# Performance work log

Measured on AMD Instinct MI355X. Metric: run time of the kernel, lower is better.

Reference implementation:

```python
import jax, jax.numpy as jnp
import numpy as np

HEADS = 16
HEAD_DIM = 64
DIM = 1024
INNER = HEADS * HEAD_DIM
EPS = 1e-5


def setup_inputs() -> dict:
    key = jax.random.key(0)
    ks = jax.random.split(key, 7)
    s_qkv = (2.0 / (DIM + 3 * INNER)) ** 0.5
    s_out = (2.0 / (INNER + DIM)) ** 0.5
    return {
        "x": jax.random.normal(ks[0], (4, 2048, DIM), dtype=jnp.float32),
        "w_qkv": jax.random.normal(ks[1], (DIM, 3 * INNER), dtype=jnp.float32) * s_qkv,
        "b_qkv": jnp.zeros((3 * INNER,), dtype=jnp.float32),
        "w_out": jax.random.normal(ks[2], (INNER, DIM), dtype=jnp.float32) * s_out,
        "b_out": jnp.zeros((DIM,), dtype=jnp.float32),
        "ln_gamma": jnp.ones((DIM,), dtype=jnp.float32),
        "ln_beta": jnp.zeros((DIM,), dtype=jnp.float32),
    }


def reference(x, w_qkv, b_qkv, w_out, b_out, ln_gamma, ln_beta):
    # Pre-norm LayerNorm
    mu = jnp.mean(x, axis=-1, keepdims=True)
    var = jnp.var(x, axis=-1, keepdims=True)
    xn = (x - mu) * jax.lax.rsqrt(var + EPS) * ln_gamma + ln_beta
    # QKV projection: [b, l, 3*inner]
    qkv = xn @ w_qkv + b_qkv
    q, k, v = jnp.split(qkv, 3, axis=-1)
    b, l, _ = x.shape
    def heads(t):  # [b, l, inner] -> [b, h, l, d]
        return t.reshape(b, l, HEADS, HEAD_DIM).transpose(0, 2, 1, 3)
    q, k, v = heads(q), heads(k), heads(v)
    scale = HEAD_DIM ** -0.5
    scores = jnp.einsum('bhqd,bhkd->bhqk', q, k) * scale
    att = jax.nn.softmax(scores, axis=-1)
    out = jnp.einsum('bhqk,bhkd->bhqd', att, v)
    out = out.transpose(0, 2, 1, 3).reshape(b, l, INNER)
    return out @ w_out + b_out
```

## Files before the change

kernel.cpp:

```cpp
#include <hip/hip_runtime.h>
#include <stdint.h>

typedef __bf16 bf16;
typedef bf16 bf16x4 __attribute__((ext_vector_type(4)));
typedef bf16 bf16x8 __attribute__((ext_vector_type(8)));
typedef float f32x4 __attribute__((ext_vector_type(4)));


__device__ __forceinline__ void gll16(const bf16* g, const bf16* l) {
  __builtin_amdgcn_global_load_lds(
      (__attribute__((address_space(1))) void*)(g),
      (__attribute__((address_space(3))) void*)(l),
      16, 0, 0);
}

__global__ __launch_bounds__(256) void prep_kernel(
    const float* __restrict__ wqkv, bf16* __restrict__ wqkvT,
    const float* __restrict__ wout, bf16* __restrict__ woutT,
    const float* __restrict__ x, const float* __restrict__ gamma,
    const float* __restrict__ beta, bf16* __restrict__ xn)
{
  __shared__ bf16 tile[32][33];
  __shared__ float red[8];
  const int bid = blockIdx.x;
  const int t = threadIdx.x;
  if (bid < 4096) {
    const int bx = bid & 127, by = bid >> 7;
    const float* in;
    bf16* out;
    int Cc, c0;
    if (bx < 96) { in = wqkv; out = wqkvT; Cc = 3072; c0 = bx * 32; }
    else         { in = wout; out = woutT; Cc = 1024; c0 = (bx - 96) * 32; }
    const int r0 = by * 32;
    const int tx = t & 31, ty = t >> 5;
#pragma unroll
    for (int i = 0; i < 32; i += 8)
      tile[ty + i][tx] = (bf16)in[(long)(r0 + ty + i) * Cc + c0 + tx];
    __syncthreads();
#pragma unroll
    for (int i = 0; i < 32; i += 8)
      out[(long)(c0 + ty + i) * 1024 + r0 + tx] = tile[tx][ty + i];
  } else {
    const long row = bid - 4096;
    f32x4 f = *(const f32x4*)(x + row * 1024 + t * 4);
    float sum = f[0] + f[1] + f[2] + f[3];
    float sq  = f[0]*f[0] + f[1]*f[1] + f[2]*f[2] + f[3]*f[3];
#pragma unroll
    for (int sh = 1; sh < 64; sh <<= 1) {
      sum += __shfl_xor(sum, sh, 64);
      sq  += __shfl_xor(sq,  sh, 64);
    }
    const int wave = t >> 6, lane = t & 63;
    if (lane == 0) { red[wave] = sum; red[wave + 4] = sq; }
    __syncthreads();
    sum = red[0] + red[1] + red[2] + red[3];
    sq  = red[4] + red[5] + red[6] + red[7];
    const float mu  = sum * (1.0f / 1024.0f);
    const float var = sq * (1.0f / 1024.0f) - mu * mu;
    const float rs  = rsqrtf(var + 1e-5f);
    f32x4 g = *(const f32x4*)(gamma + t * 4);
    f32x4 bb = *(const f32x4*)(beta + t * 4);
    bf16x4 ov;
#pragma unroll
    for (int i = 0; i < 4; i++)
      ov[i] = (bf16)((f[i] - mu) * rs * g[i] + bb[i]);
    *(bf16x4*)(xn + row * 1024 + t * 4) = ov;
  }
}

__global__ __launch_bounds__(256, 4) void gemm_bt(
    const bf16* __restrict__ A, const bf16* __restrict__ BT,
    const float* __restrict__ bias, float* __restrict__ C,
    bf16* __restrict__ qb, bf16* __restrict__ kb, bf16* __restrict__ vb,
    int K, int N, int mode)
{
  __shared__ bf16 sA[2][128 * 32];
  __shared__ bf16 sB[2][128 * 32];
  const int t = threadIdx.x;
  const int lane = t & 63;
  const int wave = t >> 6;
  const int wave_u = __builtin_amdgcn_readfirstlane(wave);
  const int quad = lane >> 4;
  const int c16 = lane & 15;
  const int wm = (wave >> 1) * 64;
  const int wn = (wave & 1) * 64;
  const int m0 = blockIdx.x * 128;
  const int n0 = blockIdx.y * 128;

  f32x4 acc[4][4] = {};

  const int srow = t >> 2;
  const int scol = (((t & 3) ^ ((t >> 3) & 3)) * 8);
  const bf16* gA = A + (long)(m0 + srow) * K + scol;
  const bf16* gB = BT + (long)(n0 + srow) * K + scol;
  const long rowskip = (long)64 * K;
  const int ksw = (quad ^ ((c16 >> 1) & 3)) * 8;

  const int S = K >> 5;

  auto stage = [&](int b, int kk) {
    const bf16* lA = sA[0] + b * 4096 + wave_u * 512;
    const bf16* lB = sB[0] + b * 4096 + wave_u * 512;
    const int k0 = kk * 32;
    gll16(gA + k0, lA);
    gll16(gA + k0 + rowskip, lA + 2048);
    gll16(gB + k0, lB);
    gll16(gB + k0 + rowskip, lB + 2048);
  };

  stage(0, 0);

  int cur = 0;
  for (int s = 0; s < S; s++) {
    __syncthreads();
    if (s + 1 < S)
      stage(cur ^ 1, s + 1);
    const bf16* cA = sA[0] + cur * 4096;
    const bf16* cB = sB[0] + cur * 4096;
    bf16x8 af[4], bfr[4];
#pragma unroll
    for (int i = 0; i < 4; i++)
      af[i] = *(const bf16x8*)(cA + (wm + i * 16 + c16) * 32 + ksw);
#pragma unroll
    for (int j = 0; j < 4; j++)
      bfr[j] = *(const bf16x8*)(cB + (wn + j * 16 + c16) * 32 + ksw);
#pragma unroll
    for (int i = 0; i < 4; i++)
#pragma unroll
      for (int j = 0; j < 4; j++)
        acc[i][j] = __builtin_amdgcn_mfma_f32_16x16x32_bf16(af[i], bfr[j], acc[i][j], 0, 0, 0);
    cur ^= 1;
  }

#pragma unroll
  for (int i = 0; i < 4; i++) {
    const int mbase = m0 + wm + i * 16 + quad * 4;
#pragma unroll
    for (int j = 0; j < 4; j++) {
      const int n = n0 + wn + j * 16 + c16;
      const float bv = bias[n];
      if (mode == 0) {
#pragma unroll
        for (int r = 0; r < 4; r++)
          C[(long)(mbase + r) * N + n] = acc[i][j][r] + bv;
      } else {
        const int part = n >> 10;
        const int inner = n & 1023;
        const int h = inner >> 6, d = inner & 63;
        bf16* dst = (part == 0) ? qb : (part == 1) ? kb : vb;
        const float scl = (part == 0) ? 0.18033688f : 1.0f;
#pragma unroll
        for (int r = 0; r < 4; r++) {
          const int m = mbase + r;
          const int b = m >> 11, l = m & 2047;
          const long bh = (long)((b << 4) | h);
          dst[(bh * 2048 + l) * 64 + d] = (bf16)((acc[i][j][r] + bv) * scl);
        }
      }
    }
  }
}

__global__ __launch_bounds__(256, 2) void attn_kernel(
    const bf16* __restrict__ q, const bf16* __restrict__ k,
    const bf16* __restrict__ vb, bf16* __restrict__ att)
{
  __shared__ bf16 sK[128 * 68];
  __shared__ bf16 sVt[64 * 132];

  const int i = blockIdx.x;
  const int xcd = i & 7;
  const int wi = i >> 3;
  const int qt = wi & 7;
  const int bh = xcd * 8 + (wi >> 3);
  const int b = bh >> 4, h = bh & 15;
  const int q0 = qt * 256;
  const int t = threadIdx.x;
  const int wave = t >> 6, lane = t & 63;
  const int quad = lane >> 4, c16 = lane & 15;

  const bf16* qp = q + (long)bh * (2048 * 64);
  const bf16* kp = k + (long)bh * (2048 * 64);
  const bf16* vp = vb + (long)bh * (2048 * 64);

  bf16x8 aq[4][2];
#pragma unroll
  for (int m = 0; m < 4; m++) {
    const bf16* qrow = qp + (long)(q0 + wave * 64 + m * 16 + c16) * 64 + quad * 8;
    aq[m][0] = *(const bf16x8*)(qrow);
    aq[m][1] = *(const bf16x8*)(qrow + 32);
  }

  f32x4 o_acc[4][4] = {};
  f32x4 o_sum[4] = {};
  bf16x8 vones;
#pragma unroll
  for (int z = 0; z < 8; z++) vones[z] = (bf16)1.0f;

  const int kr = t >> 3;
  const int kd = (t & 7) * 8;
  const int lr = t >> 1;
  const int dh = (t & 1) * 32;
  const int l32 = lr & 31;
  const int pcol = (lr >> 5) * 32 + ((l32 >> 2) & 3) * 8 + (l32 >> 4) * 4 + (l32 & 3);

  bf16x8 kreg[4], vreg[4];
#pragma unroll
  for (int it = 0; it < 4; it++)
    kreg[it] = *(const bf16x8*)(kp + (long)(it * 32 + kr) * 64 + kd);
#pragma unroll
  for (int c = 0; c < 4; c++)
    vreg[c] = *(const bf16x8*)(vp + (long)lr * 64 + dh + c * 8);

  for (int kt = 0; kt < 16; kt++) {
    __syncthreads();
#pragma unroll
    for (int it = 0; it < 4; it++)
      *(bf16x8*)&sK[(it * 32 + kr) * 68 + kd] = kreg[it];
#pragma unroll
    for (int c = 0; c < 4; c++)
#pragma unroll
      for (int u = 0; u < 8; u++)
        sVt[(dh + c * 8 + u) * 132 + pcol] = vreg[c][u];
    __syncthreads();

    const int kvn = ((kt + 1) & 15) * 128;

#pragma unroll
    for (int ks = 0; ks < 4; ks++) {
      bf16x8 ap[4];
#pragma unroll
      for (int e = 0; e < 2; e++) {
        const int jb = ks * 2 + e;
        const bf16x8 bk0 = *(const bf16x8*)&sK[(jb * 16 + c16) * 68 + quad * 8];
        const bf16x8 bk1 = *(const bf16x8*)&sK[(jb * 16 + c16) * 68 + 32 + quad * 8];
#pragma unroll
        for (int m = 0; m < 4; m++) {
          f32x4 z = {};
          z = __builtin_amdgcn_mfma_f32_16x16x32_bf16(bk0, aq[m][0], z, 0, 0, 0);
          z = __builtin_amdgcn_mfma_f32_16x16x32_bf16(bk1, aq[m][1], z, 0, 0, 0);
#pragma unroll
          for (int r = 0; r < 4; r++)
            ap[m][e * 4 + r] = (bf16)__builtin_amdgcn_exp2f(z[r]);
        }
      }
      if (ks == 1) {
#pragma unroll
        for (int it = 0; it < 4; it++)
          kreg[it] = *(const bf16x8*)(kp + (long)(kvn + it * 32 + kr) * 64 + kd);
      }
      if (ks == 2) {
#pragma unroll
        for (int c = 0; c < 4; c++)
          vreg[c] = *(const bf16x8*)(vp + (long)(kvn + lr) * 64 + dh + c * 8);
      }
      __builtin_amdgcn_s_setprio(1);
#pragma unroll
      for (int m = 0; m < 4; m++)
        o_sum[m] = __builtin_amdgcn_mfma_f32_16x16x32_bf16(ap[m], vones, o_sum[m], 0, 0, 0);
#pragma unroll
      for (int jd = 0; jd < 4; jd++) {
        const bf16x8 bv = *(const bf16x8*)&sVt[(jd * 16 + c16) * 132 + ks * 32 + quad * 8];
#pragma unroll
        for (int m = 0; m < 4; m++)
          o_acc[m][jd] = __builtin_amdgcn_mfma_f32_16x16x32_bf16(ap[m], bv, o_acc[m][jd], 0, 0, 0);
      }
      __builtin_amdgcn_s_setprio(0);
    }
  }

#pragma unroll
  for (int m = 0; m < 4; m++) {
#pragma unroll
    for (int r = 0; r < 4; r++) {
      const float inv = 1.0f / o_sum[m][r];
      const long rowbase = ((long)b * 2048 + q0 + wave * 64 + m * 16 + quad * 4 + r) * 1024 + h * 64;
#pragma unroll
      for (int jd = 0; jd < 4; jd++)
        att[rowbase + jd * 16 + c16] = (bf16)(o_acc[m][jd][r] * inv);
    }
  }
}

extern "C" void kernel_launch(void* const* d_in, const int* in_sizes, int n_in,
                              void* d_out, int out_size, void* d_ws, size_t ws_size,
                              hipStream_t stream) {
  (void)in_sizes; (void)n_in; (void)out_size; (void)ws_size;
  const float* x     = (const float*)d_in[0];
  const float* w_qkv = (const float*)d_in[1];
  const float* b_qkv = (const float*)d_in[2];
  const float* w_out = (const float*)d_in[3];
  const float* b_out = (const float*)d_in[4];
  const float* gamma = (const float*)d_in[5];
  const float* beta  = (const float*)d_in[6];
  float* out = (float*)d_out;
  bf16* ws  = (bf16*)d_ws;

  bf16* xn    = ws;
  bf16* wqkvT = ws + 8388608;
  bf16* woutT = wqkvT + 3145728;
  bf16* qbuf  = woutT + 1048576;
  bf16* kbuf  = qbuf + 8388608;
  bf16* att   = xn;
  bf16* vb    = (bf16*)d_out;

  prep_kernel<<<dim3(12288), 256, 0, stream>>>(w_qkv, wqkvT, w_out, woutT,
                                               x, gamma, beta, xn);
  gemm_bt<<<dim3(8192 / 128, 3072 / 128), 256, 0, stream>>>(
      xn, wqkvT, b_qkv, (float*)nullptr, qbuf, kbuf, vb, 1024, 3072, 1);
  attn_kernel<<<dim3(512), 256, 0, stream>>>(qbuf, kbuf, vb, att);
  gemm_bt<<<dim3(8192 / 128, 1024 / 128), 256, 0, stream>>>(
      att, woutT, b_out, out, (bf16*)nullptr, (bf16*)nullptr, (bf16*)nullptr, 1024, 1024, 0);
}
```

Before: 256.3 us.

## Double-buffer K/V shared-memory tiles in attention kernel to halve barriers

```diff
diff --git a/kernel.cpp b/kernel.cpp
--- a/kernel.cpp
+++ b/kernel.cpp
@@ -165,8 +165,8 @@
     const bf16* __restrict__ q, const bf16* __restrict__ k,
     const bf16* __restrict__ vb, bf16* __restrict__ att)
 {
-  __shared__ bf16 sK[128 * 68];
-  __shared__ bf16 sVt[64 * 132];
+  __shared__ bf16 sK[2][128 * 68];
+  __shared__ bf16 sVt[2][64 * 132];
 
   const int i = blockIdx.x;
   const int xcd = i & 7;
@@ -205,26 +205,36 @@
   const int pcol = (lr >> 5) * 32 + ((l32 >> 2) & 3) * 8 + (l32 >> 4) * 4 + (l32 & 3);
 
   bf16x8 kreg[4], vreg[4];
-#pragma unroll
-  for (int it = 0; it < 4; it++)
-    kreg[it] = *(const bf16x8*)(kp + (long)(it * 32 + kr) * 64 + kd);
-#pragma unroll
-  for (int c = 0; c < 4; c++)
-    vreg[c] = *(const bf16x8*)(vp + (long)lr * 64 + dh + c * 8);
+  auto load_k = [&](int tt) {
+#pragma unroll
+    for (int it = 0; it < 4; it++)
+      kreg[it] = *(const bf16x8*)(kp + (long)(tt * 128 + it * 32 + kr) * 64 + kd);
+  };
+  auto load_v = [&](int tt) {
+#pragma unroll
+    for (int c = 0; c < 4; c++)
+      vreg[c] = *(const bf16x8*)(vp + (long)(tt * 128 + lr) * 64 + dh + c * 8);
+  };
+  auto write_tiles = [&](int bb) {
+#pragma unroll
+    for (int it = 0; it < 4; it++)
+      *(bf16x8*)&sK[bb][(it * 32 + kr) * 68 + kd] = kreg[it];
+#pragma unroll
+    for (int c = 0; c < 4; c++)
+#pragma unroll
+      for (int u = 0; u < 8; u++)
+        sVt[bb][(dh + c * 8 + u) * 132 + pcol] = vreg[c][u];
+  };
+
+  load_k(0); load_v(0);
+  write_tiles(0);
+  load_k(1); load_v(1);
+  __syncthreads();
 
   for (int kt = 0; kt < 16; kt++) {
-    __syncthreads();
-#pragma unroll
-    for (int it = 0; it < 4; it++)
-      *(bf16x8*)&sK[(it * 32 + kr) * 68 + kd] = kreg[it];
-#pragma unroll
-    for (int c = 0; c < 4; c++)
-#pragma unroll
-      for (int u = 0; u < 8; u++)
-        sVt[(dh + c * 8 + u) * 132 + pcol] = vreg[c][u];
-    __syncthreads();
-
-    const int kvn = ((kt + 1) & 15) * 128;
+    const int p = kt & 1;
+    if (kt < 15)
+      write_tiles(p ^ 1);
 
 #pragma unroll
     for (int ks = 0; ks < 4; ks++) {
@@ -232,8 +242,8 @@
 #pragma unroll
       for (int e = 0; e < 2; e++) {
         const int jb = ks * 2 + e;
-        const bf16x8 bk0 = *(const bf16x8*)&sK[(jb * 16 + c16) * 68 + quad * 8];
-        const bf16x8 bk1 = *(const bf16x8*)&sK[(jb * 16 + c16) * 68 + 32 + quad * 8];
+        const bf16x8 bk0 = *(const bf16x8*)&sK[p][(jb * 16 + c16) * 68 + quad * 8];
+        const bf16x8 bk1 = *(const bf16x8*)&sK[p][(jb * 16 + c16) * 68 + 32 + quad * 8];
 #pragma unroll
         for (int m = 0; m < 4; m++) {
           f32x4 z = {};
@@ -244,29 +254,22 @@
             ap[m][e * 4 + r] = (bf16)__builtin_amdgcn_exp2f(z[r]);
         }
       }
-      if (ks == 1) {
-#pragma unroll
-        for (int it = 0; it < 4; it++)
-          kreg[it] = *(const bf16x8*)(kp + (long)(kvn + it * 32 + kr) * 64 + kd);
-      }
-      if (ks == 2) {
-#pragma unroll
-        for (int c = 0; c < 4; c++)
-          vreg[c] = *(const bf16x8*)(vp + (long)(kvn + lr) * 64 + dh + c * 8);
-      }
+      if (ks == 1 && kt < 14) load_k(kt + 2);
+      if (ks == 2 && kt < 14) load_v(kt + 2);
       __builtin_amdgcn_s_setprio(1);
 #pragma unroll
       for (int m = 0; m < 4; m++)
         o_sum[m] = __builtin_amdgcn_mfma_f32_16x16x32_bf16(ap[m], vones, o_sum[m], 0, 0, 0);
 #pragma unroll
       for (int jd = 0; jd < 4; jd++) {
-        const bf16x8 bv = *(const bf16x8*)&sVt[(jd * 16 + c16) * 132 + ks * 32 + quad * 8];
+        const bf16x8 bv = *(const bf16x8*)&sVt[p][(jd * 16 + c16) * 132 + ks * 32 + quad * 8];
 #pragma unroll
         for (int m = 0; m < 4; m++)
           o_acc[m][jd] = __builtin_amdgcn_mfma_f32_16x16x32_bf16(ap[m], bv, o_acc[m][jd], 0, 0, 0);
       }
       __builtin_amdgcn_s_setprio(0);
     }
+    __syncthreads();
   }
 
 #pragma unroll
```

Result: no change. 257.3 us (+0.4%).
